# Optimization experiments

Hardware: AMD Instinct MI355X
Metric: run time of the kernel (lower is better)

Reference implementation:

```python
import jax, jax.numpy as jnp
import numpy as np

PC_MIN = jnp.array([0.0, -39.68, -3.0], jnp.float32)
VOX = jnp.array([0.16, 0.16, 4.0], jnp.float32)
NX, NY = 432, 496  # grid cells in x and y (z grid size is 1)
MAXP = 32          # max points per pillar


def setup_inputs():
    key = jax.random.key(0)
    ks = jax.random.split(key, 16)
    B, N = 2, 16000
    u = jax.random.uniform(ks[0], (B, N, 4), dtype=jnp.float32)
    # points uniformly spread over the point-cloud range, intensity in [0,1)
    points = jnp.stack([u[..., 0] * 69.12, u[..., 1] * 79.36 - 39.68,
                        u[..., 2] * 4.0 - 3.0, u[..., 3]], axis=-1)

    def cw(k, co, ci):
        return jax.random.normal(k, (co, ci, 3, 3), jnp.float32) / np.float32(np.sqrt(ci * 9.0))

    def cws(k, L, c):
        return jax.random.normal(k, (L, c, c, 3, 3), jnp.float32) / np.float32(np.sqrt(c * 9.0))

    def st(k, shape):
        k1, k2 = jax.random.split(k)
        return (1.0 + 0.1 * jax.random.normal(k1, shape, jnp.float32),
                0.1 * jax.random.normal(k2, shape, jnp.float32))

    vfe_w = 0.1 * jax.random.normal(ks[1], (64, 10), jnp.float32)
    vfe_s, vfe_t = st(ks[2], (64,))
    b1_w0 = cw(ks[3], 4, 64);   b1_s0, b1_t0 = st(ks[4], (4,))
    b1_w = cws(ks[5], 3, 4);    b1_s, b1_t = st(ks[6], (3, 4))
    b2_w0 = cw(ks[7], 16, 4);   b2_s0, b2_t0 = st(ks[8], (16,))
    b2_w = cws(ks[9], 5, 16);   b2_s, b2_t = st(ks[10], (5, 16))
    b3_w0 = cw(ks[11], 64, 16); b3_s0, b3_t0 = st(ks[12], (64,))
    b3_w = cws(ks[13], 5, 64);  b3_s, b3_t = st(ks[14], (5, 64))
    return dict(points=points, vfe_w=vfe_w, vfe_s=vfe_s, vfe_t=vfe_t,
                b1_w0=b1_w0, b1_s0=b1_s0, b1_t0=b1_t0, b1_w=b1_w, b1_s=b1_s, b1_t=b1_t,
                b2_w0=b2_w0, b2_s0=b2_s0, b2_t0=b2_t0, b2_w=b2_w, b2_s=b2_s, b2_t=b2_t,
                b3_w0=b3_w0, b3_s0=b3_s0, b3_t0=b3_t0, b3_w=b3_w, b3_s=b3_s, b3_t=b3_t)


def _voxelize_vfe_scatter(points, vfe_w, vfe_s, vfe_t):
    """Hard voxelization (hash-bucket by pillar coord, pad to MAXP) + PillarVFE + scatter to BEV canvas."""
    B, N, C = points.shape
    V = B * N  # worst case: every point its own pillar
    pts = points.reshape(V, C)
    cid = jnp.floor((pts[:, :3] - PC_MIN) / VOX).astype(jnp.int32)
    cid = jnp.clip(cid, 0, jnp.array([NX - 1, NY - 1, 0], jnp.int32))
    bidx = jnp.repeat(jnp.arange(B, dtype=jnp.int32), N)
    # linear pillar id: b*NY*NX + y*NX + x  (z grid dim is 1 -> z idx always 0)
    gid = bidx * (NY * NX) + cid[:, 1] * NX + cid[:, 0]
    order = jnp.argsort(gid)  # stable -> preserves per-pillar point order
    g = gid[order]; p = pts[order]; c = cid[order]
    pos = jnp.arange(V, dtype=jnp.int32)
    flag = jnp.concatenate([jnp.ones((1,), bool), g[1:] != g[:-1]])
    vidx = jnp.cumsum(flag) - 1                                 # dense pillar index
    rank = pos - jax.lax.cummax(jnp.where(flag, pos, 0), axis=0)  # slot within pillar
    keep = rank < MAXP
    voxels = jnp.zeros((V, MAXP, C), points.dtype).at[vidx, rank].set(p, mode='drop')
    num = jnp.zeros((V,), jnp.int32).at[vidx].add(keep.astype(jnp.int32))
    OOB = B * NY * NX
    pillar_gid = jnp.full((V,), OOB, jnp.int32).at[vidx].set(g)  # unused slots stay out-of-bounds
    pillar_c = jnp.zeros((V, 3), jnp.int32).at[vidx].set(c)
    # PillarVFE features: [x,y,z,r, cluster offset(3), center offset(3)] = 10
    denom = jnp.maximum(num, 1).astype(points.dtype)[:, None]
    mean = jnp.zeros((V, 3), points.dtype).at[vidx].add(p[:, :3] * keep[:, None]) / denom
    f_cluster = voxels[:, :, :3] - mean[:, None, :]
    center = pillar_c.astype(points.dtype) * VOX + (VOX * 0.5 + PC_MIN)
    f_center = voxels[:, :, :3] - center[:, None, :]
    mask = (jnp.arange(MAXP)[None, :] < num[:, None])[:, :, None].astype(points.dtype)
    feat = jnp.concatenate([voxels, f_cluster, f_center], axis=-1) * mask  # (V, 32, 10)
    x = jnp.einsum('vpc,oc->vpo', feat, vfe_w)        # PFN linear (no bias)
    x = jax.nn.relu(x * vfe_s + vfe_t)                # eval-mode BN folded to scale/shift
    pillar = x.max(axis=1)                            # (V, 64) max over points
    canvas = jnp.zeros((B * NY * NX, 64), points.dtype).at[pillar_gid].set(pillar, mode='drop')
    return canvas.reshape(B, NY, NX, 64).transpose(0, 3, 1, 2)  # (B, 64, NY, NX)


def _conv_bn_relu(x, w, s, t):
    y = jax.lax.conv_general_dilated(x, w, (1, 1), [(1, 1), (1, 1)],
                                     dimension_numbers=('NCHW', 'OIHW', 'NCHW'))
    return jax.nn.relu(y * s[None, :, None, None] + t[None, :, None, None])


def _block(x, w0, s0, t0, ws, ss, ts):
    x = _conv_bn_relu(x, w0, s0, t0)
    for i in range(ws.shape[0]):  # fixed small layer count
        x = _conv_bn_relu(x, ws[i], ss[i], ts[i])
    return x


def reference(points, vfe_w, vfe_s, vfe_t,
              b1_w0, b1_s0, b1_t0, b1_w, b1_s, b1_t,
              b2_w0, b2_s0, b2_t0, b2_w, b2_s, b2_t,
              b3_w0, b3_s0, b3_t0, b3_w, b3_s, b3_t):
    bev = _voxelize_vfe_scatter(points, vfe_w, vfe_s, vfe_t)
    x1 = _block(bev, b1_w0, b1_s0, b1_t0, b1_w, b1_s, b1_t)
    x2 = _block(x1, b2_w0, b2_s0, b2_t0, b2_w, b2_s, b2_t)
    x3 = _block(x2, b3_w0, b3_s0, b3_t0, b3_w, b3_s, b3_t)
    # no deblocks (cfg lacks UPSAMPLE_STRIDES) -> concat raw block outputs: 4+16+64 = 84 ch
    return jnp.concatenate([x1, x2, x3], axis=1)  # (B, 84, 496, 432)
```

## Files before the change

kernel.cpp:

```cpp
#include <hip/hip_runtime.h>
#include <math.h>

static constexpr int H = 496, W = 432, Bn = 2, Np = 16000;
static constexpr int HW = H * W;

typedef __bf16 bf16x8 __attribute__((ext_vector_type(8)));
typedef float f32x16 __attribute__((ext_vector_type(16)));

__device__ inline void bin_xy(float px, float py, int& ix, int& iy) {
  ix = (int)floorf(px * 6.25f);
  iy = (int)floorf((py + 39.68f) * 6.25f);
  ix = min(max(ix, 0), W - 1);
  iy = min(max(iy, 0), H - 1);
}

__global__ __launch_bounds__(256)
void count_kernel(const float* __restrict__ pts, int* __restrict__ cnt,
                  float* __restrict__ sums) {
  int p = blockIdx.x * blockDim.x + threadIdx.x;
  if (p >= Bn * Np) return;
  float px = pts[p * 4 + 0], py = pts[p * 4 + 1], pz = pts[p * 4 + 2];
  int b = p / Np;
  int ix, iy;
  bin_xy(px, py, ix, iy);
  int gid = b * HW + iy * W + ix;
  atomicAdd(&cnt[gid], 1);
  atomicAdd(&sums[3 * gid + 0], px);
  atomicAdd(&sums[3 * gid + 1], py);
  atomicAdd(&sums[3 * gid + 2], pz);
}

__global__ __launch_bounds__(256)
void vfe_kernel(const float* __restrict__ pts, const int* __restrict__ cnt,
                const float* __restrict__ sums, const float* __restrict__ vw,
                const float* __restrict__ vs, const float* __restrict__ vt,
                float* __restrict__ canv) {
  int tid = blockIdx.x * blockDim.x + threadIdx.x;
  if (tid >= Bn * Np * 64) return;
  int o = tid & 63;
  int p = tid >> 6;
  int b = p / Np;
  float px = pts[p * 4 + 0], py = pts[p * 4 + 1];
  float pz = pts[p * 4 + 2], pr = pts[p * 4 + 3];
  int ix, iy;
  bin_xy(px, py, ix, iy);
  int gid = b * HW + iy * W + ix;
  int n = cnt[gid];
  float denom = (float)max(n, 1);
  float mx = sums[3 * gid + 0] / denom;
  float my = sums[3 * gid + 1] / denom;
  float mz = sums[3 * gid + 2] / denom;
  float cx = (float)ix * 0.16f + 0.08f;
  float cy = (float)iy * 0.16f + (0.08f - 39.68f);
  float f[10] = {px, py, pz, pr, px - mx, py - my, pz - mz,
                 px - cx, py - cy, pz + 1.0f};
  const float* wr = vw + o * 10;
  float d = 0.f;
#pragma unroll
  for (int c = 0; c < 10; c++) d += f[c] * wr[c];
  float val = d * vs[o] + vt[o];
  val = fmaxf(val, 0.f);
  if (n < 32) val = fmaxf(val, fmaxf(vt[o], 0.f));
  unsigned int* dst = (unsigned int*)(canv + (size_t)gid * 64 + o);
  atomicMax(dst, __float_as_uint(val));
}

__global__ __launch_bounds__(256, 3)
void conv64_tile(const float* __restrict__ canv, const float* __restrict__ w0,
                 const float* __restrict__ s, const float* __restrict__ t,
                 float* __restrict__ out4) {
  constexpr int PADP = 68;
  __shared__ __align__(16) float hl[180 * PADP];
  __shared__ __align__(16) float wl[4 * 576];

  const int tid = threadIdx.x;
  const int b = blockIdx.y;
  const int ty = blockIdx.x / 27, tx = blockIdx.x - ty * 27;
  const int y0 = ty * 8, x0 = tx * 16;
  const float* cb = canv + (size_t)b * HW * 64;

  for (int e = tid; e < 2304; e += 256) {
    int co = e / 576, r = e - co * 576;
    int tp = r >> 6, ci = r & 63;
    wl[e] = w0[co * 576 + ci * 9 + tp];
  }
  for (int q = tid; q < 180 * 16; q += 256) {
    int hp = q >> 4, c4 = q & 15;
    int hy = hp / 18, hx = hp - hy * 18;
    int gy = y0 - 1 + hy, gx = x0 - 1 + hx;
    float4 v = {0.f, 0.f, 0.f, 0.f};
    if ((unsigned)gy < (unsigned)H && (unsigned)gx < (unsigned)W)
      v = *(const float4*)(cb + (size_t)(gy * W + gx) * 64 + c4 * 4);
    *(float4*)(hl + hp * PADP + c4 * 4) = v;
  }
  __syncthreads();

  const int p = tid >> 1, hf = tid & 1;
  const int ly = p >> 4, lx = p & 15;
  const int co = hf * 2;
  float a0 = 0.f, a1 = 0.f;
  const float* wl0 = wl + co * 576;
  const float* wl1 = wl + (co + 1) * 576;

#pragma unroll 1
  for (int tp = 0; tp < 9; ++tp) {
    const float* hp_ = hl + ((ly + tp / 3) * 18 + lx + tp % 3) * PADP;
    const float* w0p = wl0 + tp * 64;
    const float* w1p = wl1 + tp * 64;
#pragma unroll 4
    for (int c4 = 0; c4 < 16; ++c4) {
      float4 v = *(const float4*)(hp_ + c4 * 4);
      float4 wa = *(const float4*)(w0p + c4 * 4);
      float4 wb = *(const float4*)(w1p + c4 * 4);
      a0 = fmaf(v.x, wa.x, a0);
      a1 = fmaf(v.x, wb.x, a1);
      a0 = fmaf(v.y, wa.y, a0);
      a1 = fmaf(v.y, wb.y, a1);
      a0 = fmaf(v.z, wa.z, a0);
      a1 = fmaf(v.z, wb.z, a1);
      a0 = fmaf(v.w, wa.w, a0);
      a1 = fmaf(v.w, wb.w, a1);
    }
  }
  float* ob = out4 + (size_t)b * 4 * HW + (size_t)(y0 + ly) * W + x0 + lx;
  ob[(size_t)co * HW] = fmaxf(a0 * s[co] + t[co], 0.f);
  ob[(size_t)(co + 1) * HW] = fmaxf(a1 * s[co + 1] + t[co + 1], 0.f);
}

template <int CI, int COT>
__global__ __launch_bounds__(256)
void conv3x3(const float* __restrict__ in, int in_bs, const float* __restrict__ w,
             const float* __restrict__ s, const float* __restrict__ t,
             float* __restrict__ out, int out_bs, int npix) {
  int pix = blockIdx.x * blockDim.x + threadIdx.x;
  if (pix >= npix) return;
  int b = pix / HW;
  int rem = pix - b * HW;
  int y = rem / W;
  int x = rem - y * W;
  int co0 = blockIdx.y * COT;
  const float* inb = in + (size_t)b * in_bs;

  int offs[9];
  bool okm[9];
#pragma unroll
  for (int ky = 0; ky < 3; ky++) {
    int yy = y + ky - 1;
    bool yok = (unsigned)yy < (unsigned)H;
#pragma unroll
    for (int kx = 0; kx < 3; kx++) {
      int xx = x + kx - 1;
      okm[ky * 3 + kx] = yok && ((unsigned)xx < (unsigned)W);
      offs[ky * 3 + kx] = yy * W + xx;
    }
  }
  float acc[COT];
#pragma unroll
  for (int i = 0; i < COT; i++) acc[i] = 0.f;
  for (int ci = 0; ci < CI; ci++) {
    const float* ip = inb + (size_t)ci * HW;
    float iv[9];
#pragma unroll
    for (int k = 0; k < 9; k++) iv[k] = okm[k] ? ip[offs[k]] : 0.f;
    const float* wp = w + ((size_t)co0 * CI + ci) * 9;
#pragma unroll
    for (int cg_ = 0; cg_ < COT; cg_++) {
      const float* wc = wp + (size_t)cg_ * CI * 9;
#pragma unroll
      for (int k = 0; k < 9; k++) acc[cg_] = fmaf(iv[k], wc[k], acc[cg_]);
    }
  }
  float* ob = out + (size_t)b * out_bs + (size_t)rem;
#pragma unroll
  for (int cg_ = 0; cg_ < COT; cg_++) {
    float v = acc[cg_] * s[co0 + cg_] + t[co0 + cg_];
    ob[(size_t)(co0 + cg_) * HW] = fmaxf(v, 0.f);
  }
}

__global__ __launch_bounds__(256)
void conv16_dual(const float* __restrict__ in, const float* __restrict__ w,
                 const float* __restrict__ s, const float* __restrict__ t,
                 float* __restrict__ out, __bf16* __restrict__ n16) {
  int pix = blockIdx.x * blockDim.x + threadIdx.x;
  if (pix >= Bn * HW) return;
  int b = pix / HW;
  int rem = pix - b * HW;
  int y = rem / W;
  int x = rem - y * W;
  const float* inb = in + (size_t)b * 16 * HW;

  int offs[9];
  bool okm[9];
#pragma unroll
  for (int ky = 0; ky < 3; ky++) {
    int yy = y + ky - 1;
    bool yok = (unsigned)yy < (unsigned)H;
#pragma unroll
    for (int kx = 0; kx < 3; kx++) {
      int xx = x + kx - 1;
      okm[ky * 3 + kx] = yok && ((unsigned)xx < (unsigned)W);
      offs[ky * 3 + kx] = yy * W + xx;
    }
  }
  float acc[16];
#pragma unroll
  for (int i = 0; i < 16; i++) acc[i] = 0.f;
  for (int ci = 0; ci < 16; ci++) {
    const float* ip = inb + (size_t)ci * HW;
    float iv[9];
#pragma unroll
    for (int k = 0; k < 9; k++) iv[k] = okm[k] ? ip[offs[k]] : 0.f;
    const float* wp = w + (size_t)ci * 9;
#pragma unroll
    for (int cg_ = 0; cg_ < 16; cg_++) {
      const float* wc = wp + (size_t)cg_ * 16 * 9;
#pragma unroll
      for (int k = 0; k < 9; k++) acc[cg_] = fmaf(iv[k], wc[k], acc[cg_]);
    }
  }
  float* ob = out + (size_t)b * 84 * HW + (size_t)rem;
  __bf16 vv[16];
#pragma unroll
  for (int cg_ = 0; cg_ < 16; cg_++) {
    float v = fmaxf(acc[cg_] * s[cg_] + t[cg_], 0.f);
    ob[(size_t)cg_ * HW] = v;
    vv[cg_] = (__bf16)v;
  }
  __bf16* nb = n16 + (size_t)b * (84 * HW * 2) + (size_t)rem * 16;
  *(bf16x8*)nb = *(bf16x8*)vv;
  *(bf16x8*)(nb + 8) = *(bf16x8*)(vv + 8);
}

__global__ __launch_bounds__(256)
void prepack(const float* __restrict__ w0, const float* __restrict__ ws,
             __bf16* __restrict__ wt) {
  int idx = blockIdx.x * 256 + threadIdx.x;
  const int E0 = 64 * 144, EN = 64 * 576;
  if (idx < E0) {
    int blk = idx >> 9, rem = idx & 511;
    int tp = blk >> 1, nt = blk & 1;
    int co = nt * 32 + (rem >> 4);
    int ci = rem & 15;
    int ky = tp / 3, kx = tp - ky * 3;
    wt[idx] = (__bf16)w0[((co * 16 + ci) * 3 + ky) * 3 + kx];
  } else {
    int j = idx - E0;
    if (j >= 5 * EN) return;
    int n = j / EN, rr = j - n * EN;
    int blk = rr >> 9, rem = rr & 511;
    int tpkc = blk >> 1, nt = blk & 1;
    int tp = tpkc >> 2, kc = tpkc & 3;
    int co = nt * 32 + (rem >> 4);
    int ci = kc * 16 + (rem & 15);
    int ky = tp / 3, kx = tp - ky * 3;
    wt[idx] = (__bf16)ws[n * 36864 + ((co * 64 + ci) * 3 + ky) * 3 + kx];
  }
}

template <int CI, bool FINAL>
__global__ __launch_bounds__(256, 3)
void mconv(const __bf16* __restrict__ in, size_t in_bstride,
           const __bf16* __restrict__ wt, const float* __restrict__ s,
           const float* __restrict__ t, __bf16* __restrict__ outb,
           size_t outb_bstride, float* __restrict__ outf, size_t outf_bstride) {
  constexpr int KC = CI / 16;
  constexpr int PADW = (CI == 64) ? 72 : 24;
  constexpr int HALO_B = 324 * PADW * 2;
  constexpr int TRAN_B = FINAL ? 128 * 66 * 4 : 0;
  constexpr int SMEM_B = HALO_B > TRAN_B ? HALO_B : TRAN_B;
  __shared__ __align__(16) char smem[SMEM_B];
  __bf16* hl = (__bf16*)smem;

  const int tid = threadIdx.x;
  const int bz = blockIdx.y;
  const int ty = blockIdx.x / 27, tx = blockIdx.x - ty * 27;
  const int y0 = ty * 16, x0 = tx * 16;
  in += (size_t)bz * in_bstride;

  constexpr int NCH = CI / 8;
  constexpr int TOT = 324 * NCH;
  for (int q = tid; q < TOT; q += 256) {
    int hp = q / NCH, c8 = q - hp * NCH;
    int hy = hp / 18, hx = hp - hy * 18;
    int gy = y0 - 1 + hy, gx = x0 - 1 + hx;
    int4 v = {0, 0, 0, 0};
    if ((unsigned)gy < (unsigned)H && (unsigned)gx < (unsigned)W)
      v = *(const int4*)(in + (size_t)(gy * W + gx) * CI + c8 * 8);
    *(int4*)(hl + hp * PADW + c8 * 8) = v;
  }
  __syncthreads();

  const int lane = tid & 63;
  const int wv = tid >> 6;
  const int col = lane & 31, half = lane >> 5;
  const int ly0 = 4 * wv + (col >> 4);
  const int lx = col & 15;

  f32x16 z = {0.f, 0.f, 0.f, 0.f, 0.f, 0.f, 0.f, 0.f,
              0.f, 0.f, 0.f, 0.f, 0.f, 0.f, 0.f, 0.f};
  f32x16 a00 = z, a01 = z, a10 = z, a11 = z;

  const int laneoff = col * 16 + half * 8;
  const __bf16* wbase = wt + laneoff;

#pragma unroll
  for (int tp = 0; tp < 9; ++tp) {
    const __bf16* a0r = hl + ((ly0 + tp / 3) * 18 + lx + tp % 3) * PADW + half * 8;
    const __bf16* a1r = a0r + 2 * 18 * PADW;
    const __bf16* bb = wbase + ((tp * KC) << 10);
#pragma unroll
    for (int kc = 0; kc < KC; ++kc) {
      bf16x8 af0 = *(const bf16x8*)(a0r + kc * 16);
      bf16x8 af1 = *(const bf16x8*)(a1r + kc * 16);
      bf16x8 b0 = *(const bf16x8*)(bb + (kc << 10));
      bf16x8 b1 = *(const bf16x8*)(bb + (kc << 10) + 512);
      a00 = __builtin_amdgcn_mfma_f32_32x32x16_bf16(af0, b0, a00, 0, 0, 0);
      a01 = __builtin_amdgcn_mfma_f32_32x32x16_bf16(af0, b1, a01, 0, 0, 0);
      a10 = __builtin_amdgcn_mfma_f32_32x32x16_bf16(af1, b0, a10, 0, 0, 0);
      a11 = __builtin_amdgcn_mfma_f32_32x32x16_bf16(af1, b1, a11, 0, 0, 0);
    }
  }

  float s0 = s[col], t0v = t[col], s1 = s[col + 32], t1v = t[col + 32];
  if constexpr (!FINAL) {
    __bf16* ob = outb + (size_t)bz * outb_bstride;
#pragma unroll
    for (int r = 0; r < 16; ++r) {
      int row = (r & 3) + 8 * (r >> 2) + 4 * half;
      int py = y0 + 4 * wv + (row >> 4);
      int px = x0 + (row & 15);
      size_t gp0 = (size_t)py * W + px;
      size_t gp1 = gp0 + (size_t)2 * W;
      ob[gp0 * 64 + col] = (__bf16)fmaxf(a00[r] * s0 + t0v, 0.f);
      ob[gp0 * 64 + col + 32] = (__bf16)fmaxf(a01[r] * s1 + t1v, 0.f);
      ob[gp1 * 64 + col] = (__bf16)fmaxf(a10[r] * s0 + t0v, 0.f);
      ob[gp1 * 64 + col + 32] = (__bf16)fmaxf(a11[r] * s1 + t1v, 0.f);
    }
  } else {
    float* of = outf + (size_t)bz * outf_bstride;
    float* tl = (float*)smem;
    for (int h = 0; h < 2; ++h) {
      __syncthreads();
      if ((wv >> 1) == h) {
        int wl_ = wv & 1;
#pragma unroll
        for (int r = 0; r < 16; ++r) {
          int row = (r & 3) + 8 * (r >> 2) + 4 * half;
          int lp0 = (4 * wl_ + (row >> 4)) * 16 + (row & 15);
          int lp1 = lp0 + 32;
          tl[lp0 * 66 + col] = fmaxf(a00[r] * s0 + t0v, 0.f);
          tl[lp0 * 66 + col + 32] = fmaxf(a01[r] * s1 + t1v, 0.f);
          tl[lp1 * 66 + col] = fmaxf(a10[r] * s0 + t0v, 0.f);
          tl[lp1 * 66 + col + 32] = fmaxf(a11[r] * s1 + t1v, 0.f);
        }
      }
      __syncthreads();
      for (int e = tid; e < 128 * 64; e += 256) {
        int co = e >> 7, mtl = e & 127;
        of[(size_t)co * HW + (size_t)(y0 + h * 8 + (mtl >> 4)) * W +
           (x0 + (mtl & 15))] = tl[mtl * 66 + co];
      }
    }
  }
}

extern "C" void kernel_launch(void* const* d_in, const int* in_sizes, int n_in,
                              void* d_out, int out_size, void* d_ws, size_t ws_size,
                              hipStream_t stream) {
  const float* pts  = (const float*)d_in[0];
  const float* vw   = (const float*)d_in[1];
  const float* vs   = (const float*)d_in[2];
  const float* vt   = (const float*)d_in[3];
  const float* b1w0 = (const float*)d_in[4];
  const float* b1s0 = (const float*)d_in[5];
  const float* b1t0 = (const float*)d_in[6];
  const float* b1w  = (const float*)d_in[7];
  const float* b1s  = (const float*)d_in[8];
  const float* b1t  = (const float*)d_in[9];
  const float* b2w0 = (const float*)d_in[10];
  const float* b2s0 = (const float*)d_in[11];
  const float* b2t0 = (const float*)d_in[12];
  const float* b2w  = (const float*)d_in[13];
  const float* b2s  = (const float*)d_in[14];
  const float* b2t  = (const float*)d_in[15];
  const float* b3w0 = (const float*)d_in[16];
  const float* b3s0 = (const float*)d_in[17];
  const float* b3t0 = (const float*)d_in[18];
  const float* b3w  = (const float*)d_in[19];
  const float* b3s  = (const float*)d_in[20];
  const float* b3t  = (const float*)d_in[21];
  float* out = (float*)d_out;

  float* wsf = (float*)d_ws;
  int* cnt = (int*)wsf;
  float* sums = wsf + (size_t)2 * HW;
  float* s16a = wsf;
  float* s16b = wsf + (size_t)32 * HW;
  float* canv = wsf + (size_t)64 * HW;
  __bf16* ppA = (__bf16*)d_ws;
  __bf16* Wt = (__bf16*)((char*)d_ws + (size_t)192 * HW * 4);

  prepack<<<756, 256, 0, stream>>>(b3w0, b3w, Wt);

  hipMemsetAsync(cnt, 0, (size_t)8 * HW * sizeof(float), stream);
  hipMemsetAsync(canv, 0, (size_t)128 * HW * sizeof(float), stream);

  count_kernel<<<(Bn * Np + 255) / 256, 256, 0, stream>>>(pts, cnt, sums);
  vfe_kernel<<<(Bn * Np * 64 + 255) / 256, 256, 0, stream>>>(pts, cnt, sums, vw, vs,
                                                             vt, canv);

  const int g2 = (2 * HW + 255) / 256;
  dim3 blk(256);

  conv64_tile<<<dim3(27 * 62, Bn), blk, 0, stream>>>(canv, b1w0, b1s0, b1t0, s16a);
  conv3x3<4, 4><<<dim3(g2, 1), blk, 0, stream>>>(s16a, 4 * HW, b1w + 0 * 144,
                                                 b1s + 0, b1t + 0, s16b, 4 * HW,
                                                 2 * HW);
  conv3x3<4, 4><<<dim3(g2, 1), blk, 0, stream>>>(s16b, 4 * HW, b1w + 1 * 144,
                                                 b1s + 4, b1t + 4, s16a, 4 * HW,
                                                 2 * HW);
  conv3x3<4, 4><<<dim3(g2, 1), blk, 0, stream>>>(s16a, 4 * HW, b1w + 2 * 144,
                                                 b1s + 8, b1t + 8, out, 84 * HW,
                                                 2 * HW);

  __bf16* n16 = (__bf16*)(out + (size_t)20 * HW);
  conv3x3<4, 16><<<dim3(g2, 1), blk, 0, stream>>>(out, 84 * HW, b2w0, b2s0, b2t0,
                                                  s16a, 16 * HW, 2 * HW);
  conv3x3<16, 16><<<dim3(g2, 1), blk, 0, stream>>>(s16a, 16 * HW, b2w + 0 * 2304,
                                                   b2s + 0, b2t + 0, s16b, 16 * HW,
                                                   2 * HW);
  conv3x3<16, 16><<<dim3(g2, 1), blk, 0, stream>>>(s16b, 16 * HW, b2w + 1 * 2304,
                                                   b2s + 16, b2t + 16, s16a, 16 * HW,
                                                   2 * HW);
  conv3x3<16, 16><<<dim3(g2, 1), blk, 0, stream>>>(s16a, 16 * HW, b2w + 2 * 2304,
                                                   b2s + 32, b2t + 32, s16b, 16 * HW,
                                                   2 * HW);
  conv3x3<16, 16><<<dim3(g2, 1), blk, 0, stream>>>(s16b, 16 * HW, b2w + 3 * 2304,
                                                   b2s + 48, b2t + 48, s16a, 16 * HW,
                                                   2 * HW);
  conv16_dual<<<g2, blk, 0, stream>>>(s16a, b2w + 4 * 2304, b2s + 64, b2t + 64,
                                      out + 4 * HW, n16);

  const size_t canv_s = (size_t)84 * HW * 2;
  const size_t ppa_s = (size_t)64 * HW;
  dim3 mg(31 * 27, Bn);
  mconv<16, false><<<mg, blk, 0, stream>>>(n16, canv_s, Wt, b3s0, b3t0, ppA, ppa_s,
                                           nullptr, 0);
  mconv<64, false><<<mg, blk, 0, stream>>>(ppA, ppa_s, Wt + 9216 + 0 * 36864,
                                           b3s + 0, b3t + 0, n16, canv_s, nullptr,
                                           0);
  mconv<64, false><<<mg, blk, 0, stream>>>(n16, canv_s, Wt + 9216 + 1 * 36864,
                                           b3s + 64, b3t + 64, ppA, ppa_s, nullptr,
                                           0);
  mconv<64, false><<<mg, blk, 0, stream>>>(ppA, ppa_s, Wt + 9216 + 2 * 36864,
                                           b3s + 128, b3t + 128, n16, canv_s,
                                           nullptr, 0);
  mconv<64, false><<<mg, blk, 0, stream>>>(n16, canv_s, Wt + 9216 + 3 * 36864,
                                           b3s + 192, b3t + 192, ppA, ppa_s,
                                           nullptr, 0);
  mconv<64, true><<<mg, blk, 0, stream>>>(ppA, ppa_s, Wt + 9216 + 4 * 36864,
                                          b3s + 256, b3t + 256, nullptr, 0,
                                          out + (size_t)20 * HW, (size_t)84 * HW);
}
```

Before: 821.0 us.

## Restructure first 64-channel conv: one thread per pixel, global prepacked weights, swizzled halo

```diff
diff --git a/kernel.cpp b/kernel.cpp
--- a/kernel.cpp
+++ b/kernel.cpp
@@ -65,13 +65,11 @@
   atomicMax(dst, __float_as_uint(val));
 }
 
-__global__ __launch_bounds__(256, 3)
-void conv64_tile(const float* __restrict__ canv, const float* __restrict__ w0,
+__global__ __launch_bounds__(128, 2)
+void conv64_tile(const float* __restrict__ canv, const float* __restrict__ wc,
                  const float* __restrict__ s, const float* __restrict__ t,
                  float* __restrict__ out4) {
-  constexpr int PADP = 68;
-  __shared__ __align__(16) float hl[180 * PADP];
-  __shared__ __align__(16) float wl[4 * 576];
+  __shared__ __align__(16) float hl[180 * 64];
 
   const int tid = threadIdx.x;
   const int b = blockIdx.y;
@@ -79,52 +77,55 @@
   const int y0 = ty * 8, x0 = tx * 16;
   const float* cb = canv + (size_t)b * HW * 64;
 
-  for (int e = tid; e < 2304; e += 256) {
-    int co = e / 576, r = e - co * 576;
-    int tp = r >> 6, ci = r & 63;
-    wl[e] = w0[co * 576 + ci * 9 + tp];
-  }
-  for (int q = tid; q < 180 * 16; q += 256) {
+  for (int q = tid; q < 180 * 16; q += 128) {
     int hp = q >> 4, c4 = q & 15;
     int hy = hp / 18, hx = hp - hy * 18;
     int gy = y0 - 1 + hy, gx = x0 - 1 + hx;
     float4 v = {0.f, 0.f, 0.f, 0.f};
     if ((unsigned)gy < (unsigned)H && (unsigned)gx < (unsigned)W)
       v = *(const float4*)(cb + (size_t)(gy * W + gx) * 64 + c4 * 4);
-    *(float4*)(hl + hp * PADP + c4 * 4) = v;
+    *(float4*)(hl + hp * 64 + ((c4 + hp) & 15) * 4) = v;
   }
   __syncthreads();
 
-  const int p = tid >> 1, hf = tid & 1;
-  const int ly = p >> 4, lx = p & 15;
-  const int co = hf * 2;
-  float a0 = 0.f, a1 = 0.f;
-  const float* wl0 = wl + co * 576;
-  const float* wl1 = wl + (co + 1) * 576;
+  const int ly = tid >> 4, lx = tid & 15;
+  float a0 = 0.f, a1 = 0.f, a2 = 0.f, a3 = 0.f;
 
 #pragma unroll 1
   for (int tp = 0; tp < 9; ++tp) {
-    const float* hp_ = hl + ((ly + tp / 3) * 18 + lx + tp % 3) * PADP;
-    const float* w0p = wl0 + tp * 64;
-    const float* w1p = wl1 + tp * 64;
+    const int hp = (ly + tp / 3) * 18 + lx + tp % 3;
+    const float* hb = hl + hp * 64;
+    const float* wt_ = wc + tp * 256;
 #pragma unroll 4
     for (int c4 = 0; c4 < 16; ++c4) {
-      float4 v = *(const float4*)(hp_ + c4 * 4);
-      float4 wa = *(const float4*)(w0p + c4 * 4);
-      float4 wb = *(const float4*)(w1p + c4 * 4);
-      a0 = fmaf(v.x, wa.x, a0);
-      a1 = fmaf(v.x, wb.x, a1);
-      a0 = fmaf(v.y, wa.y, a0);
-      a1 = fmaf(v.y, wb.y, a1);
-      a0 = fmaf(v.z, wa.z, a0);
-      a1 = fmaf(v.z, wb.z, a1);
-      a0 = fmaf(v.w, wa.w, a0);
-      a1 = fmaf(v.w, wb.w, a1);
+      float4 v = *(const float4*)(hb + ((c4 + hp) & 15) * 4);
+      float4 wq0 = *(const float4*)(wt_ + (c4 * 4 + 0) * 4);
+      float4 wq1 = *(const float4*)(wt_ + (c4 * 4 + 1) * 4);
+      float4 wq2 = *(const float4*)(wt_ + (c4 * 4 + 2) * 4);
+      float4 wq3 = *(const float4*)(wt_ + (c4 * 4 + 3) * 4);
+      a0 = fmaf(v.x, wq0.x, a0);
+      a1 = fmaf(v.x, wq0.y, a1);
+      a2 = fmaf(v.x, wq0.z, a2);
+      a3 = fmaf(v.x, wq0.w, a3);
+      a0 = fmaf(v.y, wq1.x, a0);
+      a1 = fmaf(v.y, wq1.y, a1);
+      a2 = fmaf(v.y, wq1.z, a2);
+      a3 = fmaf(v.y, wq1.w, a3);
+      a0 = fmaf(v.z, wq2.x, a0);
+      a1 = fmaf(v.z, wq2.y, a1);
+      a2 = fmaf(v.z, wq2.z, a2);
+      a3 = fmaf(v.z, wq2.w, a3);
+      a0 = fmaf(v.w, wq3.x, a0);
+      a1 = fmaf(v.w, wq3.y, a1);
+      a2 = fmaf(v.w, wq3.z, a2);
+      a3 = fmaf(v.w, wq3.w, a3);
     }
   }
   float* ob = out4 + (size_t)b * 4 * HW + (size_t)(y0 + ly) * W + x0 + lx;
-  ob[(size_t)co * HW] = fmaxf(a0 * s[co] + t[co], 0.f);
-  ob[(size_t)(co + 1) * HW] = fmaxf(a1 * s[co + 1] + t[co + 1], 0.f);
+  ob[0 * HW] = fmaxf(a0 * s[0] + t[0], 0.f);
+  ob[1 * HW] = fmaxf(a1 * s[1] + t[1], 0.f);
+  ob[2 * HW] = fmaxf(a2 * s[2] + t[2], 0.f);
+  ob[3 * HW] = fmaxf(a3 * s[3] + t[3], 0.f);
 }
 
 template <int CI, int COT>
@@ -165,9 +166,9 @@
     const float* wp = w + ((size_t)co0 * CI + ci) * 9;
 #pragma unroll
     for (int cg_ = 0; cg_ < COT; cg_++) {
-      const float* wc = wp + (size_t)cg_ * CI * 9;
-#pragma unroll
-      for (int k = 0; k < 9; k++) acc[cg_] = fmaf(iv[k], wc[k], acc[cg_]);
+      const float* wc_ = wp + (size_t)cg_ * CI * 9;
+#pragma unroll
+      for (int k = 0; k < 9; k++) acc[cg_] = fmaf(iv[k], wc_[k], acc[cg_]);
     }
   }
   float* ob = out + (size_t)b * out_bs + (size_t)rem;
@@ -214,9 +215,9 @@
     const float* wp = w + (size_t)ci * 9;
 #pragma unroll
     for (int cg_ = 0; cg_ < 16; cg_++) {
-      const float* wc = wp + (size_t)cg_ * 16 * 9;
-#pragma unroll
-      for (int k = 0; k < 9; k++) acc[cg_] = fmaf(iv[k], wc[k], acc[cg_]);
+      const float* wc_ = wp + (size_t)cg_ * 16 * 9;
+#pragma unroll
+      for (int k = 0; k < 9; k++) acc[cg_] = fmaf(iv[k], wc_[k], acc[cg_]);
     }
   }
   float* ob = out + (size_t)b * 84 * HW + (size_t)rem;
@@ -234,7 +235,8 @@
 
 __global__ __launch_bounds__(256)
 void prepack(const float* __restrict__ w0, const float* __restrict__ ws,
-             __bf16* __restrict__ wt) {
+             __bf16* __restrict__ wt, const float* __restrict__ w1,
+             float* __restrict__ wc) {
   int idx = blockIdx.x * 256 + threadIdx.x;
   const int E0 = 64 * 144, EN = 64 * 576;
   if (idx < E0) {
@@ -244,9 +246,8 @@
     int ci = rem & 15;
     int ky = tp / 3, kx = tp - ky * 3;
     wt[idx] = (__bf16)w0[((co * 16 + ci) * 3 + ky) * 3 + kx];
-  } else {
+  } else if (idx < E0 + 5 * EN) {
     int j = idx - E0;
-    if (j >= 5 * EN) return;
     int n = j / EN, rr = j - n * EN;
     int blk = rr >> 9, rem = rr & 511;
     int tpkc = blk >> 1, nt = blk & 1;
@@ -255,6 +256,11 @@
     int ci = kc * 16 + (rem & 15);
     int ky = tp / 3, kx = tp - ky * 3;
     wt[idx] = (__bf16)ws[n * 36864 + ((co * 64 + ci) * 3 + ky) * 3 + kx];
+  } else if (idx < E0 + 5 * EN + 2304) {
+    int e = idx - E0 - 5 * EN;
+    int tp = e >> 8, r = e & 255;
+    int ci = r >> 2, co = r & 3;
+    wc[e] = w1[co * 576 + ci * 9 + tp];
   }
 }
 
@@ -400,8 +406,9 @@
   float* canv = wsf + (size_t)64 * HW;
   __bf16* ppA = (__bf16*)d_ws;
   __bf16* Wt = (__bf16*)((char*)d_ws + (size_t)192 * HW * 4);
-
-  prepack<<<756, 256, 0, stream>>>(b3w0, b3w, Wt);
+  float* wc64 = (float*)((char*)d_ws + (size_t)192 * HW * 4 + 512 * 1024);
+
+  prepack<<<765, 256, 0, stream>>>(b3w0, b3w, Wt, b1w0, wc64);
 
   hipMemsetAsync(cnt, 0, (size_t)8 * HW * sizeof(float), stream);
   hipMemsetAsync(canv, 0, (size_t)128 * HW * sizeof(float), stream);
@@ -413,7 +420,8 @@
   const int g2 = (2 * HW + 255) / 256;
   dim3 blk(256);
 
-  conv64_tile<<<dim3(27 * 62, Bn), blk, 0, stream>>>(canv, b1w0, b1s0, b1t0, s16a);
+  conv64_tile<<<dim3(27 * 62, Bn), dim3(128), 0, stream>>>(canv, wc64, b1s0, b1t0,
+                                                           s16a);
   conv3x3<4, 4><<<dim3(g2, 1), blk, 0, stream>>>(s16a, 4 * HW, b1w + 0 * 144,
                                                  b1s + 0, b1t + 0, s16b, 4 * HW,
                                                  2 * HW);
```

Result: no change. 818.0 us, median of 2 (-0.4%).
